# Kernel optimization log

Hardware: AMD Instinct MI355X
Metric: run time of the kernel (lower is better)

Reference implementation:

```python
import jax, jax.numpy as jnp
import numpy as np

D_MODEL = 512
N_HEADS = 8
HEAD_DIM = D_MODEL // N_HEADS          # 64
ROTARY_DIM = HEAD_DIM // 2             # 32 (rotary_frac = 0.5)
MAX_SEQ_LEN = 512
EPS = 1e-6


def _rope_tables(seq_len, dtype=jnp.float32):
    inv_freq = 1.0 / (10000.0 ** (jnp.arange(0, ROTARY_DIM, 2, dtype=jnp.float32) / ROTARY_DIM))
    t = jnp.arange(seq_len, dtype=jnp.float32)
    freqs = jnp.outer(t, inv_freq)          # (T, ROTARY_DIM//2)
    return jnp.sin(freqs).astype(dtype), jnp.cos(freqs).astype(dtype)


def _apply_rope(x, sin, cos):
    # x: (R, H, T, Dh); rotate interleaved pairs of the first ROTARY_DIM dims
    rd = ROTARY_DIM
    x1 = x[..., :rd].reshape(*x.shape[:-1], rd // 2, 2)
    x2 = x[..., rd:]
    s = sin[None, None, :, :]
    c = cos[None, None, :, :]
    a, b = x1[..., 0], x1[..., 1]
    rot = jnp.stack([a * c - b * s, a * s + b * c], axis=-1).reshape(*x.shape[:-1], rd)
    return jnp.concatenate([rot, x2], axis=-1)


def setup_inputs() -> dict:
    key = jax.random.key(0)
    ks = jax.random.split(key, 8)
    B, T, N, D = 1, 384, 128, D_MODEL
    x = jax.random.normal(ks[0], (B, T, N, D), dtype=jnp.float32)
    neuron_pad_mask = jax.random.randint(ks[1], (B, N), 0, 2, dtype=jnp.int32)
    scale = 1.0 / np.sqrt(D)
    norm_w = jnp.ones((D,), dtype=jnp.float32)
    wq = jax.random.normal(ks[2], (D, D), dtype=jnp.float32) * scale
    wk = jax.random.normal(ks[3], (D, D), dtype=jnp.float32) * scale
    wv = jax.random.normal(ks[4], (D, D), dtype=jnp.float32) * scale
    wo = jax.random.normal(ks[5], (D, D), dtype=jnp.float32) * scale
    return {"x": x, "neuron_pad_mask": neuron_pad_mask, "norm_w": norm_w,
            "wq": wq, "wk": wk, "wv": wv, "wo": wo}


def reference(x, neuron_pad_mask, norm_w, wq, wk, wv, wo):
    B, T, N, D = x.shape
    H, Dh = N_HEADS, HEAD_DIM

    # RMSNorm over d_model
    xn = x * jax.lax.rsqrt(jnp.mean(x * x, axis=-1, keepdims=True) + EPS) * norm_w

    # (B,T,N,D) -> (B*N, T, D): each neuron is an independent causal timeline
    xt = jnp.transpose(xn, (0, 2, 1, 3)).reshape(B * N, T, D)
    res = xt

    # QKV projections (Linear, no bias: x @ W^T), split into heads -> (R,H,T,Dh)
    def to_bhld(y):
        return jnp.transpose(y.reshape(B * N, T, H, Dh), (0, 2, 1, 3))

    q = to_bhld(xt @ wq.T)
    k = to_bhld(xt @ wk.T)
    v = to_bhld(xt @ wv.T)

    sin, cos = _rope_tables(T, dtype=x.dtype)
    q = _apply_rope(q, sin, cos)
    k = _apply_rope(k, sin, cos)

    # Causal SDPA per row (scale = 1/sqrt(Dh), matching F.scaled_dot_product_attention)
    scores = jnp.einsum('rhtd,rhsd->rhts', q, k) / np.sqrt(Dh).astype(x.dtype)
    causal = jnp.tril(jnp.ones((T, T), dtype=bool))
    scores = jnp.where(causal[None, None], scores, jnp.finfo(scores.dtype).min)
    attn = jax.nn.softmax(scores, axis=-1)
    out = jnp.einsum('rhts,rhsd->rhtd', attn, v)            # (R,H,T,Dh)
    out = jnp.transpose(out, (0, 2, 1, 3)).reshape(B * N, T, D)

    # Only valid (non-padded) neuron rows receive attention output (others stay 0)
    valid = (neuron_pad_mask.reshape(-1) != 0)
    out = jnp.where(valid[:, None, None], out, jnp.zeros((), dtype=out.dtype))

    out = out + res
    out = jnp.transpose(out.reshape(B, N, T, D), (0, 2, 1, 3))  # (B,T,N,D)
    return out @ wo.T
```

## Files before the change

### kernel.cpp

```cpp
#include <hip/hip_runtime.h>
#include <hip/hip_bf16.h>
#include <stdint.h>

typedef __bf16 bf16x8 __attribute__((ext_vector_type(8)));
typedef float f32x4 __attribute__((ext_vector_type(4)));

static constexpr int T_SEQ  = 384;
static constexpr int NNEUR  = 128;
static constexpr int DMODEL = 512;
static constexpr int NROWS  = NNEUR * T_SEQ;
static constexpr float ROPE_C = 0.8304820237218406f;

__device__ __forceinline__ float bf2f(unsigned short u) {
  union { unsigned int i; float f; } x; x.i = ((unsigned int)u) << 16; return x.f;
}
__device__ __forceinline__ unsigned short f2bf(float f) {
  union { float f; unsigned int i; } x; x.f = f;
  unsigned int i = x.i;
  i += 0x7FFFu + ((i >> 16) & 1u);
  return (unsigned short)(i >> 16);
}
__device__ __forceinline__ float fast_exp2(float x) {
#if __has_builtin(__builtin_amdgcn_exp2f)
  return __builtin_amdgcn_exp2f(x);
#else
  return exp2f(x);
#endif
}

__device__ __forceinline__ void async_copy16(const unsigned short* g, unsigned short* l) {
  auto gp = reinterpret_cast<const __attribute__((address_space(1))) unsigned int*>(
      reinterpret_cast<uintptr_t>(g));
  auto lp = reinterpret_cast<__attribute__((address_space(3))) unsigned int*>(
      reinterpret_cast<uintptr_t>(l));
  __builtin_amdgcn_global_load_lds(gp, lp, 16, 0, 0);
}

__global__ __launch_bounds__(256) void cvt_w_kernel(
    const float* __restrict__ w0, const float* __restrict__ w1,
    const float* __restrict__ w2, const float* __restrict__ w3,
    unsigned short* __restrict__ o0, unsigned short* __restrict__ o1,
    unsigned short* __restrict__ o2, unsigned short* __restrict__ o3)
{
  const float* w; unsigned short* o;
  switch (blockIdx.y) {
    case 0:  w = w0; o = o0; break;
    case 1:  w = w1; o = o1; break;
    case 2:  w = w2; o = o2; break;
    default: w = w3; o = o3; break;
  }
  int i = (blockIdx.x * 256 + threadIdx.x) * 4;
  float4 v = *reinterpret_cast<const float4*>(w + i);
  union { unsigned short u[4]; uint2 v2; } p;
  p.u[0] = f2bf(v.x); p.u[1] = f2bf(v.y); p.u[2] = f2bf(v.z); p.u[3] = f2bf(v.w);
  *reinterpret_cast<uint2*>(o + i) = p.v2;
}

__global__ __launch_bounds__(256) void rope_tab_kernel(float2* __restrict__ tab) {
  int idx = blockIdx.x * 256 + threadIdx.x;
  int t = idx >> 4, i = idx & 15;
  float ang = (float)t * exp2f(-(float)i * ROPE_C);
  float s, c; sincosf(ang, &s, &c);
  tab[idx] = make_float2(s, c);
}

__global__ __launch_bounds__(256) void rmsnorm_kernel(
    const float* __restrict__ x, const float* __restrict__ nw,
    unsigned short* __restrict__ xt)
{
  int wave = threadIdx.x >> 6, lane = threadIdx.x & 63;
  int rid = blockIdx.x * 4 + wave;
  int t = rid >> 7, n = rid & 127;
  const float* row = x + (size_t)rid * DMODEL;
  float4 v0 = *reinterpret_cast<const float4*>(row + lane * 8);
  float4 v1 = *reinterpret_cast<const float4*>(row + lane * 8 + 4);
  float ss = v0.x*v0.x + v0.y*v0.y + v0.z*v0.z + v0.w*v0.w
           + v1.x*v1.x + v1.y*v1.y + v1.z*v1.z + v1.w*v1.w;
  #pragma unroll
  for (int off = 32; off; off >>= 1) ss += __shfl_xor(ss, off);
  float sc = rsqrtf(ss * (1.0f / DMODEL) + 1e-6f);
  float4 w0 = *reinterpret_cast<const float4*>(nw + lane * 8);
  float4 w1 = *reinterpret_cast<const float4*>(nw + lane * 8 + 4);
  union { unsigned short u[8]; uint4 v; } p;
  p.u[0] = f2bf(v0.x * sc * w0.x); p.u[1] = f2bf(v0.y * sc * w0.y);
  p.u[2] = f2bf(v0.z * sc * w0.z); p.u[3] = f2bf(v0.w * sc * w0.w);
  p.u[4] = f2bf(v1.x * sc * w1.x); p.u[5] = f2bf(v1.y * sc * w1.y);
  p.u[6] = f2bf(v1.z * sc * w1.z); p.u[7] = f2bf(v1.w * sc * w1.w);
  *reinterpret_cast<uint4*>(xt + ((size_t)n * T_SEQ + t) * DMODEL + lane * 8) = p.v;
}

template <int MODE, typename OutT>
__global__ __launch_bounds__(512, 4) void gemm_k(
    const unsigned short* __restrict__ A,
    const unsigned short* __restrict__ B,
    OutT* __restrict__ C,
    const float2* __restrict__ tab,
    const int* __restrict__ pad)
{
  __shared__ alignas(16) unsigned short Sh[384 * 64];
  const int tid  = threadIdx.x;
  const int wave = tid >> 6, lane = tid & 63;
  const int l15  = lane & 15, quad = lane >> 4;
  const int wm = (wave >> 1) * 64, wn = (wave & 1) * 64;

  constexpr int GX = (MODE == 2) ? 8 : (MODE == 3) ? 2 : 4;
  constexpr int GY = (MODE == 3) ? 384 : 192;
  constexpr int NB = GX * GY;
  constexpr int CH = NB / 8;
  const int lin = (int)blockIdx.y * GX + (int)blockIdx.x;
  const int swz = (lin & 7) * CH + (lin >> 3);
  const int bx  = swz % GX, by = swz / GX;

  size_t m0; int n0;
  if constexpr (MODE == 3) { m0 = (size_t)bx * 256; n0 = by * 128; }
  else                     { m0 = (size_t)by * 256; n0 = bx * 128; }

  if constexpr (MODE == 2) {
    int nfirst = (int)(m0 / 384);
    int nlast  = (int)((m0 + 255) / 384);
    if (pad[nfirst] == 0 && pad[nlast] == 0) return;
  }
  if constexpr (MODE == 3) {
    if (pad[n0 / 384] == 0) return;
  }

  const int srow  = tid >> 3;
  const int schunk = (tid & 7) ^ (srow & 7);
  const unsigned short* ga = A + (m0 + srow) * 512 + schunk * 8;
  const unsigned short* gb = B + ((size_t)n0 + srow) * 512 + schunk * 8;
  unsigned short* ls = &Sh[tid * 8];

  f32x4 acc[4][4] = {};
  for (int k0 = 0; k0 < 512; k0 += 64) {
    #pragma unroll
    for (int ra = 0; ra < 4; ++ra)
      async_copy16(ga + (size_t)ra * 32768 + k0, ls + ra * 4096);
    #pragma unroll
    for (int rb = 0; rb < 2; ++rb)
      async_copy16(gb + (size_t)rb * 32768 + k0, ls + (4 + rb) * 4096);
    __syncthreads();
    #pragma unroll
    for (int kc = 0; kc < 2; ++kc) {
      const int pc = ((kc * 4 + quad) ^ (l15 & 7)) * 8;
      bf16x8 a[4], b[4];
      #pragma unroll
      for (int i = 0; i < 4; ++i)
        a[i] = *reinterpret_cast<const bf16x8*>(&Sh[(wm + i * 16 + l15) * 64 + pc]);
      #pragma unroll
      for (int j = 0; j < 4; ++j)
        b[j] = *reinterpret_cast<const bf16x8*>(&Sh[(256 + wn + j * 16 + l15) * 64 + pc]);
      #pragma unroll
      for (int i = 0; i < 4; ++i)
        #pragma unroll
        for (int j = 0; j < 4; ++j)
          acc[i][j] = __builtin_amdgcn_mfma_f32_16x16x32_bf16(a[i], b[j], acc[i][j], 0, 0, 0);
    }
    __syncthreads();
  }

  if constexpr (MODE == 3) {
    #pragma unroll
    for (int j = 0; j < 4; ++j) {
      int xbase = n0 + wn + j * 16;
      int nn    = xbase / 384;
      int bloc  = xbase - nn * 384;
      int off64 = (bloc >> 6) * 64 + ((bloc >> 4) & 3);
      #pragma unroll
      for (int i = 0; i < 4; ++i)
        #pragma unroll
        for (int r = 0; r < 4; ++r) {
          int dout = (int)m0 + wm + i * 16 + quad * 4 + r;
          C[((size_t)nn * 512 + dout) * 384 + off64 + l15 * 4] = f2bf(acc[i][j][r]);
        }
    }
  } else {
    OutT* Cb = C;
    int ncol0 = n0 + wn;
    if constexpr (MODE == 2) {
      int sec = n0 >> 9;
      Cb = C + (size_t)sec * NROWS * 512;
      ncol0 = (n0 & 511) + wn;
    }
    #pragma unroll
    for (int i = 0; i < 4; ++i) {
      #pragma unroll
      for (int r = 0; r < 4; ++r) {
        size_t grow = m0 + wm + i * 16 + quad * 4 + r;
        int t = (int)(grow % 384);
        #pragma unroll
        for (int j = 0; j < 4; ++j) {
          float v = acc[i][j][r];
          int col = ncol0 + j * 16 + l15;
          if constexpr (MODE == 2) {
            if (((ncol0 + j * 16) & 63) < 32) {
              float part = __shfl_xor(v, 1);
              float2 scv = tab[t * 16 + ((col & 63) >> 1)];
              v = (l15 & 1) ? (part * scv.x + v * scv.y)
                            : (v * scv.y - part * scv.x);
            }
            Cb[grow * 512 + col] = f2bf(v);
          } else {
            Cb[grow * 512 + col] = v;
          }
        }
      }
    }
  }
}

__global__ __launch_bounds__(256, 4) void attn_kernel(
    const unsigned short* __restrict__ qb,
    const unsigned short* __restrict__ kb,
    const unsigned short* __restrict__ vt,
    const unsigned short* __restrict__ xt,
    const int* __restrict__ pad,
    unsigned short* __restrict__ y)
{
  const int lin = (int)blockIdx.x + 6 * ((int)blockIdx.y + 8 * (int)blockIdx.z);
  const int swz = (lin & 7) * 768 + (lin >> 3);
  const int qt  = swz % 6;
  const int rem = swz / 6;
  const int h   = rem & 7;
  const int n   = rem >> 3;

  const int tid  = threadIdx.x;

  if (pad[n] == 0) {
    int tq = qt * 64 + (tid >> 2);
    int d  = h * 64 + (tid & 3) * 16;
    const uint4* src = reinterpret_cast<const uint4*>(
        &xt[((size_t)n * T_SEQ + tq) * 512 + d]);
    uint4* dst = reinterpret_cast<uint4*>(
        &y[((size_t)tq * NNEUR + n) * 512 + d]);
    dst[0] = src[0];
    dst[1] = src[1];
    return;
  }

  __shared__ alignas(16) unsigned short Qs[64 * 64];
  __shared__ alignas(16) unsigned short Ks[64 * 64];
  __shared__ alignas(16) unsigned short VTs[64 * 64];
  __shared__ alignas(16) unsigned short Ps[4][16][72];

  const int wave = tid >> 6, lane = tid & 63;
  const int l15  = lane & 15, quad = lane >> 4;
  const int lrow = lane >> 3, lchunk = (lane & 7) ^ ((lane >> 3) & 7);
  const float C2 = 0.18033688011112042f;

  const unsigned short* gq =
      qb + ((size_t)n * T_SEQ + qt * 64 + wave * 16 + lrow) * 512 + h * 64 + lchunk * 8;
  async_copy16(gq,           &Qs[(wave * 16) * 64]);
  async_copy16(gq + 8 * 512, &Qs[(wave * 16 + 8) * 64]);

  const unsigned short* gk0 =
      kb + ((size_t)n * T_SEQ + wave * 16 + lrow) * 512 + h * 64 + lchunk * 8;
  const unsigned short* gv0 =
      vt + ((size_t)n * 512 + h * 64 + wave * 16 + lrow) * 384 + lchunk * 8;

  float lsum[4] = {0.f, 0.f, 0.f, 0.f};
  f32x4 oacc[4] = {};

  for (int kt = 0; kt <= qt; ++kt) {
    async_copy16(gk0 + (size_t)(kt * 64) * 512,     &Ks[(wave * 16) * 64]);
    async_copy16(gk0 + (size_t)(kt * 64 + 8) * 512, &Ks[(wave * 16 + 8) * 64]);
    async_copy16(gv0 + kt * 64,                     &VTs[(wave * 16) * 64]);
    async_copy16(gv0 + kt * 64 + 8 * 384,           &VTs[(wave * 16 + 8) * 64]);
    __syncthreads();

    f32x4 sc4[4] = {};
    #pragma unroll
    for (int kc = 0; kc < 2; ++kc) {
      const int pc = ((kc * 4 + quad) ^ (l15 & 7)) * 8;
      bf16x8 aq = *reinterpret_cast<const bf16x8*>(&Qs[(wave * 16 + l15) * 64 + pc]);
      #pragma unroll
      for (int tc = 0; tc < 4; ++tc) {
        bf16x8 bk = *reinterpret_cast<const bf16x8*>(&Ks[(tc * 16 + l15) * 64 + pc]);
        sc4[tc] = __builtin_amdgcn_mfma_f32_16x16x32_bf16(aq, bk, sc4[tc], 0, 0, 0);
      }
    }
    const bool diag = (kt == qt);
    float ps[4][4];
    #pragma unroll
    for (int tc = 0; tc < 4; ++tc)
      #pragma unroll
      for (int r = 0; r < 4; ++r) {
        float p = fast_exp2(sc4[tc][r] * C2 - 16.0f);
        if (diag && (tc * 16 + l15 > wave * 16 + quad * 4 + r)) p = 0.f;
        lsum[r] += p;
        ps[tc][r] = p;
      }
    #pragma unroll
    for (int r = 0; r < 4; ++r) {
      union { float f; unsigned int u; } a0, a1, a2, a3;
      a0.f = ps[0][r]; a1.f = ps[1][r]; a2.f = ps[2][r]; a3.f = ps[3][r];
      uint2 pk;
      pk.x = (a1.u & 0xffff0000u) | (a0.u >> 16);
      pk.y = (a3.u & 0xffff0000u) | (a2.u >> 16);
      *reinterpret_cast<uint2*>(&Ps[wave][quad * 4 + r][l15 * 4]) = pk;
    }
    #pragma unroll
    for (int kc = 0; kc < 2; ++kc) {
      const int pc = ((kc * 4 + quad) ^ (l15 & 7)) * 8;
      bf16x8 ap = *reinterpret_cast<const bf16x8*>(&Ps[wave][l15][kc * 32 + quad * 8]);
      #pragma unroll
      for (int dt = 0; dt < 4; ++dt) {
        bf16x8 bv = *reinterpret_cast<const bf16x8*>(&VTs[(dt * 16 + l15) * 64 + pc]);
        oacc[dt] = __builtin_amdgcn_mfma_f32_16x16x32_bf16(ap, bv, oacc[dt], 0, 0, 0);
      }
    }
    __syncthreads();
  }

  float inv[4];
  #pragma unroll
  for (int r = 0; r < 4; ++r) {
    float l = lsum[r];
    l += __shfl_xor(l, 1);
    l += __shfl_xor(l, 2);
    l += __shfl_xor(l, 4);
    l += __shfl_xor(l, 8);
    inv[r] = 1.0f / l;
  }
  #pragma unroll
  for (int dt = 0; dt < 4; ++dt)
    #pragma unroll
    for (int r = 0; r < 4; ++r) {
      int tq = qt * 64 + wave * 16 + quad * 4 + r;
      int d  = h * 64 + dt * 16 + l15;
      float val = oacc[dt][r] * inv[r];
      float res = bf2f(xt[((size_t)n * T_SEQ + tq) * 512 + d]);
      y[((size_t)tq * NNEUR + n) * 512 + d] = f2bf(val + res);
    }
}

extern "C" void kernel_launch(void* const* d_in, const int* in_sizes, int n_in,
                              void* d_out, int out_size, void* d_ws, size_t ws_size,
                              hipStream_t stream) {
  const float* x   = (const float*)d_in[0];
  const int*   pad = (const int*)d_in[1];
  const float* nw  = (const float*)d_in[2];
  const float* wq  = (const float*)d_in[3];
  const float* wk  = (const float*)d_in[4];
  const float* wv  = (const float*)d_in[5];
  const float* wo  = (const float*)d_in[6];
  float* out = (float*)d_out;

  char* ws = (char*)d_ws;
  size_t off = 0;
  auto alloc = [&](size_t bytes) { void* p = ws + off; off += (bytes + 255) & ~(size_t)255; return p; };
  const size_t WELEM  = (size_t)512 * 512;
  const size_t MBYTES = (size_t)NROWS * 512 * 2;
  unsigned short* wqkv_bf = (unsigned short*)alloc(WELEM * 3 * 2);
  unsigned short* wo_bf   = (unsigned short*)alloc(WELEM * 2);
  float2*         rtab    = (float2*)alloc(384 * 16 * sizeof(float2));
  unsigned short* xt_bf   = (unsigned short*)alloc(MBYTES);
  unsigned short* qk_buf  = (unsigned short*)alloc(MBYTES * 2);
  unsigned short* vt_buf  = (unsigned short*)alloc(MBYTES);
  unsigned short* y_buf   = (unsigned short*)alloc(MBYTES);

  cvt_w_kernel<<<dim3(256, 4), 256, 0, stream>>>(
      wq, wk, wv, wo,
      wqkv_bf, wqkv_bf + WELEM, wqkv_bf + 2 * WELEM, wo_bf);
  rope_tab_kernel<<<24, 256, 0, stream>>>(rtab);
  rmsnorm_kernel<<<NROWS / 4, 256, 0, stream>>>(x, nw, xt_bf);
  gemm_k<2, unsigned short><<<dim3(8, NROWS / 256), 512, 0, stream>>>(
      xt_bf, wqkv_bf, qk_buf, rtab, pad);
  gemm_k<3, unsigned short><<<dim3(2, NROWS / 128), 512, 0, stream>>>(
      wqkv_bf + 2 * WELEM, xt_bf, vt_buf, nullptr, pad);
  attn_kernel<<<dim3(6, 8, 128), 256, 0, stream>>>(
      qk_buf, qk_buf + (size_t)NROWS * 512, vt_buf, xt_bf, pad, y_buf);
  gemm_k<0, float><<<dim3(4, NROWS / 256), 512, 0, stream>>>(
      y_buf, wo_bf, out, nullptr, nullptr);
}
```

Measured before the change: 358.2 us.

## Double-buffer GEMM LDS tiles with async prefetch of next K-slice

The GEMM main loop now keeps two LDS buffers with K-step 32. It prefetches the next K-slice through async copies while MFMAs run on the current buffer, using vmcnt waits and raw barriers instead of full syncthreads. The goal is to hide global-load latency that the old single-buffer load-sync-compute loop exposed. The trade-off is twice as many iterations, each with less compute, plus a finer swizzle. LDS use drops from 48KB to 48KB split over two 24KB buffers.

```diff
diff --git a/kernel.cpp b/kernel.cpp
--- a/kernel.cpp
+++ b/kernel.cpp
@@ -97,7 +97,7 @@
     const float2* __restrict__ tab,
     const int* __restrict__ pad)
 {
-  __shared__ alignas(16) unsigned short Sh[384 * 64];
+  __shared__ alignas(16) unsigned short Sh[2][12288];
   const int tid  = threadIdx.x;
   const int wave = tid >> 6, lane = tid & 63;
   const int l15  = lane & 15, quad = lane >> 4;
@@ -124,39 +124,56 @@
     if (pad[n0 / 384] == 0) return;
   }
 
-  const int srow  = tid >> 3;
-  const int schunk = (tid & 7) ^ (srow & 7);
-  const unsigned short* ga = A + (m0 + srow) * 512 + schunk * 8;
-  const unsigned short* gb = B + ((size_t)n0 + srow) * 512 + schunk * 8;
-  unsigned short* ls = &Sh[tid * 8];
+  const int r4 = tid >> 2;
+  const int c4 = tid & 3;
+  const int gc = c4 ^ (r4 & 3);
+  const unsigned short* ga = A + (m0 + r4) * 512 + gc * 8;
+  const unsigned short* gb = B + ((size_t)n0 + r4) * 512 + gc * 8;
+
+  const int pc = (quad ^ (l15 & 3)) * 8;
+
+  auto STAGE = [&](int kk, int b) {
+    const unsigned short* gak = ga + kk * 32;
+    unsigned short* base = &Sh[b][0];
+    async_copy16(gak,             base + tid * 8);
+    async_copy16(gak + 128 * 512, base + 4096 + tid * 8);
+    async_copy16(gb + kk * 32,    base + 8192 + tid * 8);
+  };
 
   f32x4 acc[4][4] = {};
-  for (int k0 = 0; k0 < 512; k0 += 64) {
-    #pragma unroll
-    for (int ra = 0; ra < 4; ++ra)
-      async_copy16(ga + (size_t)ra * 32768 + k0, ls + ra * 4096);
-    #pragma unroll
-    for (int rb = 0; rb < 2; ++rb)
-      async_copy16(gb + (size_t)rb * 32768 + k0, ls + (4 + rb) * 4096);
-    __syncthreads();
-    #pragma unroll
-    for (int kc = 0; kc < 2; ++kc) {
-      const int pc = ((kc * 4 + quad) ^ (l15 & 7)) * 8;
-      bf16x8 a[4], b[4];
-      #pragma unroll
-      for (int i = 0; i < 4; ++i)
-        a[i] = *reinterpret_cast<const bf16x8*>(&Sh[(wm + i * 16 + l15) * 64 + pc]);
+  auto COMPUTE = [&](int b) {
+    const unsigned short* base = &Sh[b][0];
+    bf16x8 a[4], bb[4];
+    #pragma unroll
+    for (int i = 0; i < 4; ++i)
+      a[i] = *reinterpret_cast<const bf16x8*>(&base[(wm + i * 16 + l15) * 32 + pc]);
+    #pragma unroll
+    for (int j = 0; j < 4; ++j)
+      bb[j] = *reinterpret_cast<const bf16x8*>(&base[8192 + (wn + j * 16 + l15) * 32 + pc]);
+    #pragma unroll
+    for (int i = 0; i < 4; ++i)
       #pragma unroll
       for (int j = 0; j < 4; ++j)
-        b[j] = *reinterpret_cast<const bf16x8*>(&Sh[(256 + wn + j * 16 + l15) * 64 + pc]);
-      #pragma unroll
-      for (int i = 0; i < 4; ++i)
-        #pragma unroll
-        for (int j = 0; j < 4; ++j)
-          acc[i][j] = __builtin_amdgcn_mfma_f32_16x16x32_bf16(a[i], b[j], acc[i][j], 0, 0, 0);
-    }
-    __syncthreads();
-  }
+        acc[i][j] = __builtin_amdgcn_mfma_f32_16x16x32_bf16(a[i], bb[j], acc[i][j], 0, 0, 0);
+  };
+
+  STAGE(0, 0);
+  #pragma unroll 2
+  for (int kk = 0; kk < 15; ++kk) {
+    const int b = kk & 1;
+    STAGE(kk + 1, b ^ 1);
+    asm volatile("s_waitcnt vmcnt(3)" ::: "memory");
+    __builtin_amdgcn_s_barrier();
+    __builtin_amdgcn_sched_barrier(0);
+    COMPUTE(b);
+    __builtin_amdgcn_sched_barrier(0);
+    __builtin_amdgcn_s_barrier();
+    __builtin_amdgcn_sched_barrier(0);
+  }
+  asm volatile("s_waitcnt vmcnt(0)" ::: "memory");
+  __builtin_amdgcn_s_barrier();
+  __builtin_amdgcn_sched_barrier(0);
+  COMPUTE(1);
 
   if constexpr (MODE == 3) {
     #pragma unroll
@@ -370,5 +387,5 @@
   attn_kernel<<<dim3(6, 8, 128), 256, 0, stream>>>(
       qk_buf, qk_buf + (size_t)NROWS * 512, vt_buf, xt_bf, pad, y_buf);
   gemm_k<0, float><<<dim3(4, NROWS / 256), 512, 0, stream>>>(
-      y_buf, wo_bf, out, nullptr, nullptr);
-}
+      y_buf, wo_bf, out, nullptr, pad);
+}
```

Result: no change. 352.8 us (-1.5%).
